# Kernel optimization log

Hardware: AMD Instinct MI355X
Metric: run time of the kernel (lower is better)

Reference implementation:

```python
import jax, jax.numpy as jnp
import numpy as np

NUM_ELEMENTS = 100
EMBED_DIM = 256
HIDDEN_DIM = 512
NUM_HEADS = 8
NUM_MASKS = 1
NUM_GAUSSIANS = 50
RBF_RADIUS = 12.0
N_NODES = 20000
N_EDGES = 400000


def setup_inputs() -> dict:
    key = jax.random.key(0)
    ks = jax.random.split(key, 10)
    anum = jax.random.randint(ks[0], (N_NODES,), 0, NUM_ELEMENTS)
    edge_index = jax.random.randint(ks[1], (2, N_EDGES), 0, N_NODES)
    edge_to_src = jax.random.randint(ks[2], (N_EDGES,), 0, N_EDGES)
    dist = jax.random.uniform(ks[3], (N_EDGES,), jnp.float32) * RBF_RADIUS
    # learned parameters (init scales follow reset_parameters)
    emb_table = jax.random.normal(ks[4], (NUM_ELEMENTS ** 2, EMBED_DIM), jnp.float32)
    s_gate = np.sqrt(3.0 / 2.50663)
    gate_W = jax.random.uniform(ks[5], (HIDDEN_DIM, NUM_GAUSSIANS), jnp.float32, -s_gate, s_gate)
    in_dim = EMBED_DIM + NUM_GAUSSIANS
    s_emb = np.sqrt(3.0 / EMBED_DIM)
    W_emb = jax.random.uniform(ks[6], (HIDDEN_DIM, EMBED_DIM), jnp.float32, -s_emb, s_emb)
    W_rbf = jax.random.uniform(ks[7], (HIDDEN_DIM, NUM_GAUSSIANS), jnp.float32, -s_gate, s_gate)
    W_in = jnp.concatenate([W_emb, W_rbf], axis=1)  # [H, emb+G]
    b_in = jnp.zeros((HIDDEN_DIM,), jnp.float32)
    s_out = np.sqrt(1.0 / HIDDEN_DIM)
    W_out = jax.random.uniform(ks[8], (NUM_HEADS * NUM_MASKS, HIDDEN_DIM), jnp.float32, -s_out, s_out)
    b_out = jnp.zeros((NUM_HEADS * NUM_MASKS,), jnp.float32)
    return {"anum": anum, "edge_index": edge_index, "edge_to_src": edge_to_src,
            "dist": dist, "emb_table": emb_table, "gate_W": gate_W,
            "W_in": W_in, "b_in": b_in, "W_out": W_out, "b_out": b_out}


def _gaussian_smearing(dist):
    offset = jnp.linspace(0.0, RBF_RADIUS, NUM_GAUSSIANS, dtype=dist.dtype)
    coeff = -0.5 / (offset[1] - offset[0]) ** 2
    d = dist[:, None] - offset[None, :]  # [E, G]
    return jnp.exp(coeff * d * d)


def reference(anum, edge_index, edge_to_src, dist, emb_table, gate_W, W_in, b_in, W_out, b_out):
    rbf = _gaussian_smearing(dist)                                  # [E, G]
    pair_idx = anum[edge_index[0]] + NUM_ELEMENTS * anum[edge_index[1]]  # [E]
    emb = emb_table[pair_idx]                                       # [E, D]
    x = jnp.concatenate([emb[edge_to_src], rbf], axis=-1)           # [E, D+G]
    gate = rbf @ gate_W.T                                           # [E, H]
    h = jax.nn.silu(x @ W_in.T + b_in) * gate                       # gated ResMLP hidden
    att_bias = h @ W_out.T + b_out                                  # [E, heads*masks]
    att_bias = att_bias.reshape(dist.shape[0], NUM_HEADS, NUM_MASKS)
    return jnp.transpose(att_bias, (2, 1, 0))                       # [masks, heads, E]
```

## Files before the change

kernel.cpp:

```cpp
#include <hip/hip_runtime.h>
#include <hip/hip_bf16.h>

typedef unsigned short u16;
typedef unsigned int   uint;
typedef __attribute__((ext_vector_type(8))) short bf16x8;
typedef __attribute__((ext_vector_type(4))) float f32x4;

constexpr int NELEM = 100;
constexpr int EMBED = 256;
constexpr int HID   = 512;
constexpr int KX    = 306;
constexpr int G     = 50;
constexpr int M     = 64;
constexpr int THREADS = 512;

constexpr int WB_ELEMS = 32 * 10 * 64 * 8;
constexpr int GB_ELEMS = 32 * 2 * 64 * 8;
constexpr int OB_ELEMS = 16 * 64 * 8;
constexpr int WEIGHT_ELEMS = WB_ELEMS + GB_ELEMS + OB_ELEMS;
constexpr int NPREP = WEIGHT_ELEMS / THREADS;

__device__ __forceinline__ u16 f2bf(float x) {
    uint u = __float_as_uint(x);
    u = (u + 0x7fffu + ((u >> 16) & 1u)) >> 16;
    return (u16)u;
}
__device__ __forceinline__ uint pk2(float a, float b) {
    __hip_bfloat162 h = __float22bfloat162_rn(make_float2(a, b));
    return *reinterpret_cast<uint*>(&h);
}
__device__ __forceinline__ float bflo(uint u) { return __uint_as_float(u << 16); }
__device__ __forceinline__ float bfhi(uint u) { return __uint_as_float(u & 0xffff0000u); }
__device__ __forceinline__ float silu(float p) {
    return p * __builtin_amdgcn_rcpf(1.f + __expf(-p));
}
__device__ __forceinline__ f32x4 mfma16(bf16x8 a, bf16x8 b, f32x4 c) {
    return __builtin_amdgcn_mfma_f32_16x16x32_bf16(a, b, c, 0, 0, 0);
}

__global__ __launch_bounds__(THREADS)
void prep_hist_kernel(const float* __restrict__ W_in,
                      const float* __restrict__ gate_W,
                      const float* __restrict__ W_out,
                      const float* __restrict__ b_in,
                      const int* __restrict__ anum,
                      const int* __restrict__ edge_index,
                      const int* __restrict__ edge_to_src,
                      u16* __restrict__ Wb,
                      u16* __restrict__ Gb,
                      u16* __restrict__ Ob,
                      u16* __restrict__ pairids,
                      int* __restrict__ bins,
                      int E) {
    const int bid = blockIdx.x;
    const int t   = threadIdx.x;

    if (bid < NPREP) {
        int idx = bid * THREADS + t;
        if (idx < WB_ELEMS) {
            int j = idx & 7, lane = (idx >> 3) & 63, kn = idx >> 9;
            int ks = kn % 10, nt = kn / 10;
            int h = nt * 16 + (lane & 15);
            int k = ks * 32 + (lane >> 4) * 8 + j;
            float v = (k < KX) ? W_in[h * KX + k] : ((k == KX) ? b_in[h] : 0.f);
            Wb[idx] = f2bf(v);
        } else if (idx < WB_ELEMS + GB_ELEMS) {
            int i2 = idx - WB_ELEMS;
            int j = i2 & 7, lane = (i2 >> 3) & 63, kn = i2 >> 9;
            int ks = kn & 1, nt = kn >> 1;
            int h = nt * 16 + (lane & 15);
            int g = ks * 32 + (lane >> 4) * 8 + j;
            Gb[i2] = f2bf((g < G) ? gate_W[h * G + g] : 0.f);
        } else {
            int i2 = idx - WB_ELEMS - GB_ELEMS;
            int j = i2 & 7, lane = (i2 >> 3) & 63, s = i2 >> 9;
            int m = lane & 15, q = lane >> 4;
            int hid = s * 32 + (j >> 2) * 16 + q * 4 + (j & 3);
            Ob[i2] = f2bf((m < 8) ? W_out[m * HID + hid] : 0.f);
        }
        return;
    }
    int i = (bid - NPREP) * THREADS + t;
    if (i < E) {
        int src  = edge_to_src[i];
        int pair = anum[edge_index[src]] + NELEM * anum[edge_index[E + src]];
        pairids[i] = (u16)pair;
        atomicAdd(&bins[pair], 1);
    }
}

__global__ __launch_bounds__(THREADS)
void scan_kernel(int* __restrict__ bins, int npair) {
    __shared__ int lds[THREADS];
    const int t = threadIdx.x;
    const int chunk = (npair + THREADS - 1) / THREADS;
    const int lo = t * chunk;
    const int hi = min(lo + chunk, npair);
    int s = 0;
    for (int i = lo; i < hi; ++i) s += bins[i];
    lds[t] = s;
    __syncthreads();
    for (int off = 1; off < THREADS; off <<= 1) {
        int add = (t >= off) ? lds[t - off] : 0;
        __syncthreads();
        lds[t] += add;
        __syncthreads();
    }
    int excl = lds[t] - s;
    for (int i = lo; i < hi; ++i) {
        int c = bins[i];
        bins[i] = excl;
        excl += c;
    }
}

__global__ __launch_bounds__(THREADS)
void scatter_hpre_kernel(const float* __restrict__ table,
                         const u16* __restrict__ Wb,
                         const u16* __restrict__ pairids,
                         int* __restrict__ bins,
                         int* __restrict__ perm,
                         u16* __restrict__ spair,
                         float* __restrict__ hpreF,
                         u16*   __restrict__ hpreH,
                         int E, int npair, int nsc, int f32h) {
    __shared__ __align__(16) u16 af[8 * 4 * 64 * 8];
    const int bid = blockIdx.x;
    const int t   = threadIdx.x;

    if (bid < nsc) {
        int i = bid * THREADS + t;
        if (i < E) {
            int p   = pairids[i];
            int pos = atomicAdd(&bins[p], 1);
            perm[pos]  = i;
            spair[pos] = (u16)p;
        }
        return;
    }

    const int pb = bid - nsc;
    const int p0 = pb * M;
    const int wave = t >> 6, lane = t & 63;
    const int col = lane & 15, quad = lane >> 4;

    #pragma unroll
    for (int mt = 0; mt < 4; ++mt) {
        int p = p0 + mt * 16 + col;
        uint4 w = {0u, 0u, 0u, 0u};
        if (p < npair) {
            const float* s = table + (size_t)p * EMBED + wave * 32 + quad * 8;
            float4 v0 = ((const float4*)s)[0], v1 = ((const float4*)s)[1];
            w.x = pk2(v0.x, v0.y); w.y = pk2(v0.z, v0.w);
            w.z = pk2(v1.x, v1.y); w.w = pk2(v1.z, v1.w);
        }
        *(uint4*)&af[((wave * 4 + mt) * 64 + lane) * 8] = w;
    }
    __syncthreads();

    const f32x4 z4 = {0.f, 0.f, 0.f, 0.f};
    #pragma unroll
    for (int nh = 0; nh < 2; ++nh) {
        f32x4 acc[2][4];
        #pragma unroll
        for (int ntl = 0; ntl < 2; ++ntl)
            #pragma unroll
            for (int mt = 0; mt < 4; ++mt) acc[ntl][mt] = z4;
        #pragma unroll 2
        for (int ks = 0; ks < 8; ++ks) {
            bf16x8 a[4];
            #pragma unroll
            for (int mt = 0; mt < 4; ++mt)
                a[mt] = *(const bf16x8*)&af[((ks * 4 + mt) * 64 + lane) * 8];
            #pragma unroll
            for (int ntl = 0; ntl < 2; ++ntl) {
                int ntg = wave * 4 + nh * 2 + ntl;
                bf16x8 wf = *(const bf16x8*)&Wb[((ntg * 10 + ks) * 64 + lane) * 8];
                #pragma unroll
                for (int mt = 0; mt < 4; ++mt)
                    acc[ntl][mt] = mfma16(wf, a[mt], acc[ntl][mt]);
            }
        }
        #pragma unroll
        for (int ntl = 0; ntl < 2; ++ntl)
            #pragma unroll
            for (int mt = 0; mt < 4; ++mt) {
                int p = p0 + mt * 16 + col;
                if (p < npair) {
                    int hb = (wave * 4 + nh * 2 + ntl) * 16 + quad * 4;
                    if (f32h) {
                        *(f32x4*)(hpreF + (size_t)p * HID + hb) = acc[ntl][mt];
                    } else {
                        uint2 o;
                        o.x = pk2(acc[ntl][mt][0], acc[ntl][mt][1]);
                        o.y = pk2(acc[ntl][mt][2], acc[ntl][mt][3]);
                        *(uint2*)(hpreH + (size_t)p * HID + hb) = o;
                    }
                }
            }
    }
}

template <bool F32H>
__global__ __launch_bounds__(THREADS, 4)
void pair_embed_srt(const int* __restrict__ perm,
                    const u16* __restrict__ spair,
                    const float* __restrict__ dist,
                    const float* __restrict__ hpreF,
                    const u16*   __restrict__ hpreH,
                    const float* __restrict__ b_out,
                    const u16* __restrict__ Wb,
                    const u16* __restrict__ Gb,
                    const u16* __restrict__ Ob,
                    float* __restrict__ out,
                    int E) {
    __shared__ __align__(16) u16 smem[16384];
    __shared__ int   rowbase[M];
    __shared__ float dste[M];
    __shared__ int   oidx[M];
    u16*   afrag = smem;
    float* redf  = (float*)smem;

    const int t  = threadIdx.x;
    const int e0 = blockIdx.x * M;
    const int wave = t >> 6, lane = t & 63;
    const int col = lane & 15, quad = lane >> 4;

    if (t < M) {
        int slot = e0 + t;
        int pair = 0, orig = 0; float d = 0.f;
        if (slot < E) {
            orig = perm[slot];
            pair = spair[slot];
            d    = dist[orig];
        }
        rowbase[t] = pair * HID;
        dste[t]    = d;
        oidx[t]    = orig;
    }
    __syncthreads();

    int rbm[4];
    #pragma unroll
    for (int mt = 0; mt < 4; ++mt) rbm[mt] = rowbase[mt * 16 + col];

    f32x4 hp[2][4];
    uint2 hph[2][4];
    #pragma unroll
    for (int mt = 0; mt < 4; ++mt) {
        int base = rbm[mt] + (wave * 4) * 16 + quad * 4;
        if (F32H) {
            const float* p = hpreF + base;
            hp[0][mt] = *(const f32x4*)p;
            hp[1][mt] = *(const f32x4*)(p + 16);
        } else {
            const u16* p = hpreH + base;
            hph[0][mt] = *(const uint2*)p;
            hph[1][mt] = *(const uint2*)(p + 16);
        }
    }

    {
        const float sp    = 12.0f / 49.0f;
        const float coeff = -0.5f / (sp * sp);
        int ks = wave & 1, mtr = wave >> 1;
        float d  = dste[mtr * 16 + col];
        int   g0 = ks * 32 + quad * 8;
        float f[8];
        #pragma unroll
        for (int j = 0; j < 8; ++j) {
            int g = g0 + j;
            float dd = d - sp * (float)g;
            f[j] = (g < G) ? __expf(coeff * dd * dd) : ((g == G) ? 1.f : 0.f);
        }
        uint4 w;
        w.x = pk2(f[0], f[1]); w.y = pk2(f[2], f[3]);
        w.z = pk2(f[4], f[5]); w.w = pk2(f[6], f[7]);
        *(uint4*)&afrag[((ks * 4 + mtr) * 64 + lane) * 8] = w;
    }
    __syncthreads();

    const f32x4 z4 = {0.f, 0.f, 0.f, 0.f};
    f32x4 oacc[4] = {z4, z4, z4, z4};

    #pragma unroll
    for (int nh = 0; nh < 2; ++nh) {
        if (nh == 1) {
            #pragma unroll
            for (int mt = 0; mt < 4; ++mt) {
                int base = rbm[mt] + (wave * 4 + 2) * 16 + quad * 4;
                if (F32H) {
                    const float* p = hpreF + base;
                    hp[0][mt] = *(const f32x4*)p;
                    hp[1][mt] = *(const f32x4*)(p + 16);
                } else {
                    const u16* p = hpreH + base;
                    hph[0][mt] = *(const uint2*)p;
                    hph[1][mt] = *(const uint2*)(p + 16);
                }
            }
        }
        f32x4 acc[2][4], gacc[2][4];
        #pragma unroll
        for (int ntl = 0; ntl < 2; ++ntl)
            #pragma unroll
            for (int mt = 0; mt < 4; ++mt) {
                gacc[ntl][mt] = z4;
                if (F32H) {
                    acc[ntl][mt] = hp[ntl][mt];
                } else {
                    uint2 v = hph[ntl][mt];
                    f32x4 a = {bflo(v.x), bfhi(v.x), bflo(v.y), bfhi(v.y)};
                    acc[ntl][mt] = a;
                }
            }

        const u16* gb = &Gb[((wave * 4 + nh * 2) * 2 * 64 + lane) * 8];
        const u16* wb = &Wb[(((wave * 4 + nh * 2) * 10 + 8) * 64 + lane) * 8];
        #pragma unroll
        for (int ks = 0; ks < 2; ++ks) {
            bf16x8 a[4];
            #pragma unroll
            for (int mt = 0; mt < 4; ++mt)
                a[mt] = *(const bf16x8*)&afrag[((ks * 4 + mt) * 64 + lane) * 8];
            bf16x8 g0f = *(const bf16x8*)&gb[ks * 512];
            bf16x8 w0f = *(const bf16x8*)&wb[ks * 512];
            bf16x8 g1f = *(const bf16x8*)&gb[1024 + ks * 512];
            bf16x8 w1f = *(const bf16x8*)&wb[5120 + ks * 512];
            #pragma unroll
            for (int mt = 0; mt < 4; ++mt) gacc[0][mt] = mfma16(g0f, a[mt], gacc[0][mt]);
            #pragma unroll
            for (int mt = 0; mt < 4; ++mt) acc[0][mt]  = mfma16(w0f, a[mt], acc[0][mt]);
            #pragma unroll
            for (int mt = 0; mt < 4; ++mt) gacc[1][mt] = mfma16(g1f, a[mt], gacc[1][mt]);
            #pragma unroll
            for (int mt = 0; mt < 4; ++mt) acc[1][mt]  = mfma16(w1f, a[mt], acc[1][mt]);
        }

        bf16x8 obf = *(const bf16x8*)&Ob[(((wave << 1) | nh) * 64 + lane) * 8];
        #pragma unroll
        for (int mt = 0; mt < 4; ++mt) {
            uint4 hq;
            hq.x = pk2(silu(acc[0][mt][0]) * gacc[0][mt][0],
                       silu(acc[0][mt][1]) * gacc[0][mt][1]);
            hq.y = pk2(silu(acc[0][mt][2]) * gacc[0][mt][2],
                       silu(acc[0][mt][3]) * gacc[0][mt][3]);
            hq.z = pk2(silu(acc[1][mt][0]) * gacc[1][mt][0],
                       silu(acc[1][mt][1]) * gacc[1][mt][1]);
            hq.w = pk2(silu(acc[1][mt][2]) * gacc[1][mt][2],
                       silu(acc[1][mt][3]) * gacc[1][mt][3]);
            oacc[mt] = mfma16(obf, *(bf16x8*)&hq, oacc[mt]);
        }
    }
    __syncthreads();

    #pragma unroll
    for (int mt = 0; mt < 4; ++mt)
        *(f32x4*)&redf[((wave * 4 + mt) * 64 + lane) * 4] = oacc[mt];
    __syncthreads();

    {
        int head = t >> 6, el = t & 63;
        int mt = el >> 4, c = el & 15;
        int l  = (head >> 2) * 16 + c;
        int r  = head & 3;
        float s = 0.f;
        #pragma unroll
        for (int w = 0; w < 8; ++w)
            s += redf[((w * 4 + mt) * 64 + l) * 4 + r];
        int slot = e0 + el;
        if (slot < E) out[head * E + oidx[el]] = s + b_out[head];
    }
}

template <bool F32H>
__global__ __launch_bounds__(THREADS, 4)
void pair_embed_pre(const int* __restrict__ anum,
                    const int* __restrict__ edge_index,
                    const int* __restrict__ edge_to_src,
                    const float* __restrict__ dist,
                    const float* __restrict__ hpreF,
                    const u16*   __restrict__ hpreH,
                    const float* __restrict__ b_out,
                    const u16* __restrict__ Wb,
                    const u16* __restrict__ Gb,
                    const u16* __restrict__ Ob,
                    float* __restrict__ out,
                    int E) {
    __shared__ __align__(16) u16 smem[16384];
    __shared__ int   rowbase[M];
    __shared__ float dste[M];
    u16*   afrag = smem;
    float* redf  = (float*)smem;

    const int t  = threadIdx.x;
    const int e0 = blockIdx.x * M;
    const int wave = t >> 6, lane = t & 63;
    const int col = lane & 15, quad = lane >> 4;

    if (t < M) {
        int eg = e0 + t;
        int pair = 0; float d = 0.f;
        if (eg < E) {
            int src = edge_to_src[eg];
            pair = anum[edge_index[src]] + NELEM * anum[edge_index[E + src]];
            d = dist[eg];
        }
        rowbase[t] = pair * HID;
        dste[t]    = d;
    }
    __syncthreads();

    int rbm[4];
    #pragma unroll
    for (int mt = 0; mt < 4; ++mt) rbm[mt] = rowbase[mt * 16 + col];

    f32x4 hp[2][4];
    uint2 hph[2][4];
    #pragma unroll
    for (int mt = 0; mt < 4; ++mt) {
        int base = rbm[mt] + (wave * 4) * 16 + quad * 4;
        if (F32H) {
            const float* p = hpreF + base;
            hp[0][mt] = *(const f32x4*)p;
            hp[1][mt] = *(const f32x4*)(p + 16);
        } else {
            const u16* p = hpreH + base;
            hph[0][mt] = *(const uint2*)p;
            hph[1][mt] = *(const uint2*)(p + 16);
        }
    }

    {
        const float sp    = 12.0f / 49.0f;
        const float coeff = -0.5f / (sp * sp);
        int ks = wave & 1, mtr = wave >> 1;
        float d  = dste[mtr * 16 + col];
        int   g0 = ks * 32 + quad * 8;
        float f[8];
        #pragma unroll
        for (int j = 0; j < 8; ++j) {
            int g = g0 + j;
            float dd = d - sp * (float)g;
            f[j] = (g < G) ? __expf(coeff * dd * dd) : ((g == G) ? 1.f : 0.f);
        }
        uint4 w;
        w.x = pk2(f[0], f[1]); w.y = pk2(f[2], f[3]);
        w.z = pk2(f[4], f[5]); w.w = pk2(f[6], f[7]);
        *(uint4*)&afrag[((ks * 4 + mtr) * 64 + lane) * 8] = w;
    }
    __syncthreads();

    const f32x4 z4 = {0.f, 0.f, 0.f, 0.f};
    f32x4 oacc[4] = {z4, z4, z4, z4};

    #pragma unroll
    for (int nh = 0; nh < 2; ++nh) {
        if (nh == 1) {
            #pragma unroll
            for (int mt = 0; mt < 4; ++mt) {
                int base = rbm[mt] + (wave * 4 + 2) * 16 + quad * 4;
                if (F32H) {
                    const float* p = hpreF + base;
                    hp[0][mt] = *(const f32x4*)p;
                    hp[1][mt] = *(const f32x4*)(p + 16);
                } else {
                    const u16* p = hpreH + base;
                    hph[0][mt] = *(const uint2*)p;
                    hph[1][mt] = *(const uint2*)(p + 16);
                }
            }
        }
        f32x4 acc[2][4], gacc[2][4];
        #pragma unroll
        for (int ntl = 0; ntl < 2; ++ntl)
            #pragma unroll
            for (int mt = 0; mt < 4; ++mt) {
                gacc[ntl][mt] = z4;
                if (F32H) {
                    acc[ntl][mt] = hp[ntl][mt];
                } else {
                    uint2 v = hph[ntl][mt];
                    f32x4 a = {bflo(v.x), bfhi(v.x), bflo(v.y), bfhi(v.y)};
                    acc[ntl][mt] = a;
                }
            }

        const u16* gb = &Gb[((wave * 4 + nh * 2) * 2 * 64 + lane) * 8];
        const u16* wb = &Wb[(((wave * 4 + nh * 2) * 10 + 8) * 64 + lane) * 8];
        #pragma unroll
        for (int ks = 0; ks < 2; ++ks) {
            bf16x8 a[4];
            #pragma unroll
            for (int mt = 0; mt < 4; ++mt)
                a[mt] = *(const bf16x8*)&afrag[((ks * 4 + mt) * 64 + lane) * 8];
            bf16x8 g0f = *(const bf16x8*)&gb[ks * 512];
            bf16x8 w0f = *(const bf16x8*)&wb[ks * 512];
            bf16x8 g1f = *(const bf16x8*)&gb[1024 + ks * 512];
            bf16x8 w1f = *(const bf16x8*)&wb[5120 + ks * 512];
            #pragma unroll
            for (int mt = 0; mt < 4; ++mt) gacc[0][mt] = mfma16(g0f, a[mt], gacc[0][mt]);
            #pragma unroll
            for (int mt = 0; mt < 4; ++mt) acc[0][mt]  = mfma16(w0f, a[mt], acc[0][mt]);
            #pragma unroll
            for (int mt = 0; mt < 4; ++mt) gacc[1][mt] = mfma16(g1f, a[mt], gacc[1][mt]);
            #pragma unroll
            for (int mt = 0; mt < 4; ++mt) acc[1][mt]  = mfma16(w1f, a[mt], acc[1][mt]);
        }

        bf16x8 obf = *(const bf16x8*)&Ob[(((wave << 1) | nh) * 64 + lane) * 8];
        #pragma unroll
        for (int mt = 0; mt < 4; ++mt) {
            uint4 hq;
            hq.x = pk2(silu(acc[0][mt][0]) * gacc[0][mt][0],
                       silu(acc[0][mt][1]) * gacc[0][mt][1]);
            hq.y = pk2(silu(acc[0][mt][2]) * gacc[0][mt][2],
                       silu(acc[0][mt][3]) * gacc[0][mt][3]);
            hq.z = pk2(silu(acc[1][mt][0]) * gacc[1][mt][0],
                       silu(acc[1][mt][1]) * gacc[1][mt][1]);
            hq.w = pk2(silu(acc[1][mt][2]) * gacc[1][mt][2],
                       silu(acc[1][mt][3]) * gacc[1][mt][3]);
            oacc[mt] = mfma16(obf, *(bf16x8*)&hq, oacc[mt]);
        }
    }
    __syncthreads();

    #pragma unroll
    for (int mt = 0; mt < 4; ++mt)
        *(f32x4*)&redf[((wave * 4 + mt) * 64 + lane) * 4] = oacc[mt];
    __syncthreads();

    {
        int head = t >> 6, el = t & 63;
        int mt = el >> 4, c = el & 15;
        int l  = (head >> 2) * 16 + c;
        int r  = head & 3;
        float s = 0.f;
        #pragma unroll
        for (int w = 0; w < 8; ++w)
            s += redf[((w * 4 + mt) * 64 + l) * 4 + r];
        int eg = e0 + el;
        if (eg < E) out[head * E + eg] = s + b_out[head];
    }
}

extern "C" void kernel_launch(void* const* d_in, const int* in_sizes, int n_in,
                              void* d_out, int out_size, void* d_ws, size_t ws_size,
                              hipStream_t stream) {
    const int*   anum        = (const int*)d_in[0];
    const int*   edge_index  = (const int*)d_in[1];
    const int*   edge_to_src = (const int*)d_in[2];
    const float* dist        = (const float*)d_in[3];
    const float* emb_table   = (const float*)d_in[4];
    const float* gate_W      = (const float*)d_in[5];
    const float* W_in        = (const float*)d_in[6];
    const float* b_in        = (const float*)d_in[7];
    const float* W_out       = (const float*)d_in[8];
    const float* b_out       = (const float*)d_in[9];
    const int E     = in_sizes[3];
    const int TBL   = in_sizes[4];
    const int NPAIR = TBL / EMBED;

    u16* Wb = (u16*)d_ws;
    u16* Gb = Wb + WB_ELEMS;
    u16* Ob = Gb + GB_ELEMS;
    const size_t WSW  = (size_t)WEIGHT_ELEMS * 2;
    const size_t hb32 = (size_t)NPAIR * HID * 4;
    const size_t hb16 = (size_t)NPAIR * HID * 2;
    const size_t sortx = (size_t)E * 8 + (size_t)NPAIR * 4;

    int mode;
    if      (ws_size >= WSW + hb32 + sortx) mode = 4;
    else if (ws_size >= WSW + hb16 + sortx) mode = 3;
    else if (ws_size >= WSW + hb32)         mode = 2;
    else                                    mode = 1;

    const size_t hb = (mode == 4 || mode == 2) ? hb32 : hb16;
    char*  hbase   = (char*)d_ws + WSW;
    float* hpreF   = (float*)hbase;
    u16*   hpreH   = (u16*)hbase;
    char*  q       = hbase + hb;
    int*   perm    = (int*)q;
    u16*   pairids = (u16*)(q + (size_t)E * 4);
    u16*   spair   = (u16*)(q + (size_t)E * 6);
    int*   bins    = (int*)(q + (size_t)E * 8);

    const int nhist   = (E + THREADS - 1) / THREADS;
    const int npb     = (NPAIR + M - 1) / M;
    const int nblocks = (E + M - 1) / M;
    const int f32h    = (mode == 4 || mode == 2) ? 1 : 0;

    if (mode >= 3) {
        hipMemsetAsync(bins, 0, (size_t)NPAIR * 4, stream);
        prep_hist_kernel<<<NPREP + nhist, THREADS, 0, stream>>>(
            W_in, gate_W, W_out, b_in, anum, edge_index, edge_to_src,
            Wb, Gb, Ob, pairids, bins, E);
        scan_kernel<<<1, THREADS, 0, stream>>>(bins, NPAIR);
        scatter_hpre_kernel<<<nhist + npb, THREADS, 0, stream>>>(
            emb_table, Wb, pairids, bins, perm, spair, hpreF, hpreH,
            E, NPAIR, nhist, f32h);
        if (mode == 4) {
            pair_embed_srt<true><<<nblocks, THREADS, 0, stream>>>(
                perm, spair, dist, hpreF, hpreH, b_out, Wb, Gb, Ob, (float*)d_out, E);
        } else {
            pair_embed_srt<false><<<nblocks, THREADS, 0, stream>>>(
                perm, spair, dist, hpreF, hpreH, b_out, Wb, Gb, Ob, (float*)d_out, E);
        }
    } else {
        prep_hist_kernel<<<NPREP, THREADS, 0, stream>>>(
            W_in, gate_W, W_out, b_in, anum, edge_index, edge_to_src,
            Wb, Gb, Ob, pairids, bins, E);
        scatter_hpre_kernel<<<npb, THREADS, 0, stream>>>(
            emb_table, Wb, pairids, bins, perm, spair, hpreF, hpreH,
            E, NPAIR, 0, f32h);
        if (mode == 2) {
            pair_embed_pre<true><<<nblocks, THREADS, 0, stream>>>(
                anum, edge_index, edge_to_src, dist, hpreF, hpreH,
                b_out, Wb, Gb, Ob, (float*)d_out, E);
        } else {
            pair_embed_pre<false><<<nblocks, THREADS, 0, stream>>>(
                anum, edge_index, edge_to_src, dist, hpreF, hpreH,
                b_out, Wb, Gb, Ob, (float*)d_out, E);
        }
    }
}
```

Before: 293.2 us.

## Scatter sorted distances and permute outputs in a separate coalesced pass

In the scatter pass the kernel now records each edge's sorted position and writes its distance into sorted order. The main kernel therefore reads spair and sdist contiguously instead of gathering perm and dist. The main kernel writes its results to a sorted-order scratch buffer. A new permute kernel then gathers those rows and writes the head-major output with coalesced stores, replacing the scattered per-head writes. The bf16 hpre fallback paths are removed. This costs an extra kernel launch, a scratch buffer of E*32 bytes, and extra traffic for the round trip through that buffer.

```diff
diff --git a/kernel.cpp b/kernel.cpp
--- a/kernel.cpp
+++ b/kernel.cpp
@@ -29,8 +29,6 @@
     __hip_bfloat162 h = __float22bfloat162_rn(make_float2(a, b));
     return *reinterpret_cast<uint*>(&h);
 }
-__device__ __forceinline__ float bflo(uint u) { return __uint_as_float(u << 16); }
-__device__ __forceinline__ float bfhi(uint u) { return __uint_as_float(u & 0xffff0000u); }
 __device__ __forceinline__ float silu(float p) {
     return p * __builtin_amdgcn_rcpf(1.f + __expf(-p));
 }
@@ -118,12 +116,13 @@
 void scatter_hpre_kernel(const float* __restrict__ table,
                          const u16* __restrict__ Wb,
                          const u16* __restrict__ pairids,
+                         const float* __restrict__ dist,
                          int* __restrict__ bins,
-                         int* __restrict__ perm,
+                         int* __restrict__ ip,
                          u16* __restrict__ spair,
+                         float* __restrict__ sdist,
                          float* __restrict__ hpreF,
-                         u16*   __restrict__ hpreH,
-                         int E, int npair, int nsc, int f32h) {
+                         int E, int npair, int nsc, int mode_a) {
     __shared__ __align__(16) u16 af[8 * 4 * 64 * 8];
     const int bid = blockIdx.x;
     const int t   = threadIdx.x;
@@ -133,7 +132,12 @@
         if (i < E) {
             int p   = pairids[i];
             int pos = atomicAdd(&bins[p], 1);
-            perm[pos]  = i;
+            if (mode_a) {
+                ip[i]      = pos;
+                sdist[pos] = dist[i];
+            } else {
+                ip[pos] = i;
+            }
             spair[pos] = (u16)p;
         }
         return;
@@ -188,36 +192,25 @@
                 int p = p0 + mt * 16 + col;
                 if (p < npair) {
                     int hb = (wave * 4 + nh * 2 + ntl) * 16 + quad * 4;
-                    if (f32h) {
-                        *(f32x4*)(hpreF + (size_t)p * HID + hb) = acc[ntl][mt];
-                    } else {
-                        uint2 o;
-                        o.x = pk2(acc[ntl][mt][0], acc[ntl][mt][1]);
-                        o.y = pk2(acc[ntl][mt][2], acc[ntl][mt][3]);
-                        *(uint2*)(hpreH + (size_t)p * HID + hb) = o;
-                    }
+                    *(f32x4*)(hpreF + (size_t)p * HID + hb) = acc[ntl][mt];
                 }
             }
     }
 }
 
-template <bool F32H>
 __global__ __launch_bounds__(THREADS, 4)
-void pair_embed_srt(const int* __restrict__ perm,
-                    const u16* __restrict__ spair,
-                    const float* __restrict__ dist,
-                    const float* __restrict__ hpreF,
-                    const u16*   __restrict__ hpreH,
-                    const float* __restrict__ b_out,
-                    const u16* __restrict__ Wb,
-                    const u16* __restrict__ Gb,
-                    const u16* __restrict__ Ob,
-                    float* __restrict__ out,
-                    int E) {
+void pair_embed_srtA(const u16* __restrict__ spair,
+                     const float* __restrict__ sdist,
+                     const float* __restrict__ hpreF,
+                     const float* __restrict__ b_out,
+                     const u16* __restrict__ Wb,
+                     const u16* __restrict__ Gb,
+                     const u16* __restrict__ Ob,
+                     float* __restrict__ tmp,
+                     int E) {
     __shared__ __align__(16) u16 smem[16384];
     __shared__ int   rowbase[M];
     __shared__ float dste[M];
-    __shared__ int   oidx[M];
     u16*   afrag = smem;
     float* redf  = (float*)smem;
 
@@ -228,15 +221,10 @@
 
     if (t < M) {
         int slot = e0 + t;
-        int pair = 0, orig = 0; float d = 0.f;
-        if (slot < E) {
-            orig = perm[slot];
-            pair = spair[slot];
-            d    = dist[orig];
-        }
+        int pair = 0; float d = 0.f;
+        if (slot < E) { pair = spair[slot]; d = sdist[slot]; }
         rowbase[t] = pair * HID;
         dste[t]    = d;
-        oidx[t]    = orig;
     }
     __syncthreads();
 
@@ -245,19 +233,11 @@
     for (int mt = 0; mt < 4; ++mt) rbm[mt] = rowbase[mt * 16 + col];
 
     f32x4 hp[2][4];
-    uint2 hph[2][4];
     #pragma unroll
     for (int mt = 0; mt < 4; ++mt) {
-        int base = rbm[mt] + (wave * 4) * 16 + quad * 4;
-        if (F32H) {
-            const float* p = hpreF + base;
-            hp[0][mt] = *(const f32x4*)p;
-            hp[1][mt] = *(const f32x4*)(p + 16);
-        } else {
-            const u16* p = hpreH + base;
-            hph[0][mt] = *(const uint2*)p;
-            hph[1][mt] = *(const uint2*)(p + 16);
-        }
+        const float* p = hpreF + rbm[mt] + (wave * 4) * 16 + quad * 4;
+        hp[0][mt] = *(const f32x4*)p;
+        hp[1][mt] = *(const f32x4*)(p + 16);
     }
 
     {
@@ -288,16 +268,9 @@
         if (nh == 1) {
             #pragma unroll
             for (int mt = 0; mt < 4; ++mt) {
-                int base = rbm[mt] + (wave * 4 + 2) * 16 + quad * 4;
-                if (F32H) {
-                    const float* p = hpreF + base;
-                    hp[0][mt] = *(const f32x4*)p;
-                    hp[1][mt] = *(const f32x4*)(p + 16);
-                } else {
-                    const u16* p = hpreH + base;
-                    hph[0][mt] = *(const uint2*)p;
-                    hph[1][mt] = *(const uint2*)(p + 16);
-                }
+                const float* p = hpreF + rbm[mt] + (wave * 4 + 2) * 16 + quad * 4;
+                hp[0][mt] = *(const f32x4*)p;
+                hp[1][mt] = *(const f32x4*)(p + 16);
             }
         }
         f32x4 acc[2][4], gacc[2][4];
@@ -306,13 +279,7 @@
             #pragma unroll
             for (int mt = 0; mt < 4; ++mt) {
                 gacc[ntl][mt] = z4;
-                if (F32H) {
-                    acc[ntl][mt] = hp[ntl][mt];
-                } else {
-                    uint2 v = hph[ntl][mt];
-                    f32x4 a = {bflo(v.x), bfhi(v.x), bflo(v.y), bfhi(v.y)};
-                    acc[ntl][mt] = a;
-                }
+                acc[ntl][mt]  = hp[ntl][mt];
             }
 
         const u16* gb = &Gb[((wave * 4 + nh * 2) * 2 * 64 + lane) * 8];
@@ -360,6 +327,171 @@
     __syncthreads();
 
     {
+        int el = t >> 3, head = t & 7;
+        int mt = el >> 4, c = el & 15;
+        int l  = (head >> 2) * 16 + c;
+        int r  = head & 3;
+        float s = 0.f;
+        #pragma unroll
+        for (int w = 0; w < 8; ++w)
+            s += redf[((w * 4 + mt) * 64 + l) * 4 + r];
+        int slot = e0 + el;
+        if (slot < E) tmp[slot * 8 + head] = s + b_out[head];
+    }
+}
+
+__global__ __launch_bounds__(256)
+void permute_out_kernel(const int* __restrict__ iperm,
+                        const float* __restrict__ tmp,
+                        float* __restrict__ out, int E) {
+    int e = blockIdx.x * 256 + threadIdx.x;
+    if (e < E) {
+        int s8 = iperm[e] * 8;
+        f32x4 v0 = *(const f32x4*)(tmp + s8);
+        f32x4 v1 = *(const f32x4*)(tmp + s8 + 4);
+        #pragma unroll
+        for (int h = 0; h < 4; ++h) out[h * E + e] = v0[h];
+        #pragma unroll
+        for (int h = 0; h < 4; ++h) out[(h + 4) * E + e] = v1[h];
+    }
+}
+
+__global__ __launch_bounds__(THREADS, 4)
+void pair_embed_srtB(const int* __restrict__ perm,
+                     const u16* __restrict__ spair,
+                     const float* __restrict__ dist,
+                     const float* __restrict__ hpreF,
+                     const float* __restrict__ b_out,
+                     const u16* __restrict__ Wb,
+                     const u16* __restrict__ Gb,
+                     const u16* __restrict__ Ob,
+                     float* __restrict__ out,
+                     int E) {
+    __shared__ __align__(16) u16 smem[16384];
+    __shared__ int   rowbase[M];
+    __shared__ float dste[M];
+    __shared__ int   oidx[M];
+    u16*   afrag = smem;
+    float* redf  = (float*)smem;
+
+    const int t  = threadIdx.x;
+    const int e0 = blockIdx.x * M;
+    const int wave = t >> 6, lane = t & 63;
+    const int col = lane & 15, quad = lane >> 4;
+
+    if (t < M) {
+        int slot = e0 + t;
+        int pair = 0, orig = 0; float d = 0.f;
+        if (slot < E) {
+            orig = perm[slot];
+            pair = spair[slot];
+            d    = dist[orig];
+        }
+        rowbase[t] = pair * HID;
+        dste[t]    = d;
+        oidx[t]    = orig;
+    }
+    __syncthreads();
+
+    int rbm[4];
+    #pragma unroll
+    for (int mt = 0; mt < 4; ++mt) rbm[mt] = rowbase[mt * 16 + col];
+
+    f32x4 hp[2][4];
+    #pragma unroll
+    for (int mt = 0; mt < 4; ++mt) {
+        const float* p = hpreF + rbm[mt] + (wave * 4) * 16 + quad * 4;
+        hp[0][mt] = *(const f32x4*)p;
+        hp[1][mt] = *(const f32x4*)(p + 16);
+    }
+
+    {
+        const float sp    = 12.0f / 49.0f;
+        const float coeff = -0.5f / (sp * sp);
+        int ks = wave & 1, mtr = wave >> 1;
+        float d  = dste[mtr * 16 + col];
+        int   g0 = ks * 32 + quad * 8;
+        float f[8];
+        #pragma unroll
+        for (int j = 0; j < 8; ++j) {
+            int g = g0 + j;
+            float dd = d - sp * (float)g;
+            f[j] = (g < G) ? __expf(coeff * dd * dd) : ((g == G) ? 1.f : 0.f);
+        }
+        uint4 w;
+        w.x = pk2(f[0], f[1]); w.y = pk2(f[2], f[3]);
+        w.z = pk2(f[4], f[5]); w.w = pk2(f[6], f[7]);
+        *(uint4*)&afrag[((ks * 4 + mtr) * 64 + lane) * 8] = w;
+    }
+    __syncthreads();
+
+    const f32x4 z4 = {0.f, 0.f, 0.f, 0.f};
+    f32x4 oacc[4] = {z4, z4, z4, z4};
+
+    #pragma unroll
+    for (int nh = 0; nh < 2; ++nh) {
+        if (nh == 1) {
+            #pragma unroll
+            for (int mt = 0; mt < 4; ++mt) {
+                const float* p = hpreF + rbm[mt] + (wave * 4 + 2) * 16 + quad * 4;
+                hp[0][mt] = *(const f32x4*)p;
+                hp[1][mt] = *(const f32x4*)(p + 16);
+            }
+        }
+        f32x4 acc[2][4], gacc[2][4];
+        #pragma unroll
+        for (int ntl = 0; ntl < 2; ++ntl)
+            #pragma unroll
+            for (int mt = 0; mt < 4; ++mt) {
+                gacc[ntl][mt] = z4;
+                acc[ntl][mt]  = hp[ntl][mt];
+            }
+
+        const u16* gb = &Gb[((wave * 4 + nh * 2) * 2 * 64 + lane) * 8];
+        const u16* wb = &Wb[(((wave * 4 + nh * 2) * 10 + 8) * 64 + lane) * 8];
+        #pragma unroll
+        for (int ks = 0; ks < 2; ++ks) {
+            bf16x8 a[4];
+            #pragma unroll
+            for (int mt = 0; mt < 4; ++mt)
+                a[mt] = *(const bf16x8*)&afrag[((ks * 4 + mt) * 64 + lane) * 8];
+            bf16x8 g0f = *(const bf16x8*)&gb[ks * 512];
+            bf16x8 w0f = *(const bf16x8*)&wb[ks * 512];
+            bf16x8 g1f = *(const bf16x8*)&gb[1024 + ks * 512];
+            bf16x8 w1f = *(const bf16x8*)&wb[5120 + ks * 512];
+            #pragma unroll
+            for (int mt = 0; mt < 4; ++mt) gacc[0][mt] = mfma16(g0f, a[mt], gacc[0][mt]);
+            #pragma unroll
+            for (int mt = 0; mt < 4; ++mt) acc[0][mt]  = mfma16(w0f, a[mt], acc[0][mt]);
+            #pragma unroll
+            for (int mt = 0; mt < 4; ++mt) gacc[1][mt] = mfma16(g1f, a[mt], gacc[1][mt]);
+            #pragma unroll
+            for (int mt = 0; mt < 4; ++mt) acc[1][mt]  = mfma16(w1f, a[mt], acc[1][mt]);
+        }
+
+        bf16x8 obf = *(const bf16x8*)&Ob[(((wave << 1) | nh) * 64 + lane) * 8];
+        #pragma unroll
+        for (int mt = 0; mt < 4; ++mt) {
+            uint4 hq;
+            hq.x = pk2(silu(acc[0][mt][0]) * gacc[0][mt][0],
+                       silu(acc[0][mt][1]) * gacc[0][mt][1]);
+            hq.y = pk2(silu(acc[0][mt][2]) * gacc[0][mt][2],
+                       silu(acc[0][mt][3]) * gacc[0][mt][3]);
+            hq.z = pk2(silu(acc[1][mt][0]) * gacc[1][mt][0],
+                       silu(acc[1][mt][1]) * gacc[1][mt][1]);
+            hq.w = pk2(silu(acc[1][mt][2]) * gacc[1][mt][2],
+                       silu(acc[1][mt][3]) * gacc[1][mt][3]);
+            oacc[mt] = mfma16(obf, *(bf16x8*)&hq, oacc[mt]);
+        }
+    }
+    __syncthreads();
+
+    #pragma unroll
+    for (int mt = 0; mt < 4; ++mt)
+        *(f32x4*)&redf[((wave * 4 + mt) * 64 + lane) * 4] = oacc[mt];
+    __syncthreads();
+
+    {
         int head = t >> 6, el = t & 63;
         int mt = el >> 4, c = el & 15;
         int l  = (head >> 2) * 16 + c;
@@ -373,20 +505,18 @@
     }
 }
 
-template <bool F32H>
 __global__ __launch_bounds__(THREADS, 4)
-void pair_embed_pre(const int* __restrict__ anum,
-                    const int* __restrict__ edge_index,
-                    const int* __restrict__ edge_to_src,
-                    const float* __restrict__ dist,
-                    const float* __restrict__ hpreF,
-                    const u16*   __restrict__ hpreH,
-                    const float* __restrict__ b_out,
-                    const u16* __restrict__ Wb,
-                    const u16* __restrict__ Gb,
-                    const u16* __restrict__ Ob,
-                    float* __restrict__ out,
-                    int E) {
+void pair_embed_unsrt(const int* __restrict__ anum,
+                      const int* __restrict__ edge_index,
+                      const int* __restrict__ edge_to_src,
+                      const float* __restrict__ dist,
+                      const float* __restrict__ hpreF,
+                      const float* __restrict__ b_out,
+                      const u16* __restrict__ Wb,
+                      const u16* __restrict__ Gb,
+                      const u16* __restrict__ Ob,
+                      float* __restrict__ out,
+                      int E) {
     __shared__ __align__(16) u16 smem[16384];
     __shared__ int   rowbase[M];
     __shared__ float dste[M];
@@ -416,19 +546,11 @@
     for (int mt = 0; mt < 4; ++mt) rbm[mt] = rowbase[mt * 16 + col];
 
     f32x4 hp[2][4];
-    uint2 hph[2][4];
     #pragma unroll
     for (int mt = 0; mt < 4; ++mt) {
-        int base = rbm[mt] + (wave * 4) * 16 + quad * 4;
-        if (F32H) {
-            const float* p = hpreF + base;
-            hp[0][mt] = *(const f32x4*)p;
-            hp[1][mt] = *(const f32x4*)(p + 16);
-        } else {
-            const u16* p = hpreH + base;
-            hph[0][mt] = *(const uint2*)p;
-            hph[1][mt] = *(const uint2*)(p + 16);
-        }
+        const float* p = hpreF + rbm[mt] + (wave * 4) * 16 + quad * 4;
+        hp[0][mt] = *(const f32x4*)p;
+        hp[1][mt] = *(const f32x4*)(p + 16);
     }
 
     {
@@ -459,16 +581,9 @@
         if (nh == 1) {
             #pragma unroll
             for (int mt = 0; mt < 4; ++mt) {
-                int base = rbm[mt] + (wave * 4 + 2) * 16 + quad * 4;
-                if (F32H) {
-                    const float* p = hpreF + base;
-                    hp[0][mt] = *(const f32x4*)p;
-                    hp[1][mt] = *(const f32x4*)(p + 16);
-                } else {
-                    const u16* p = hpreH + base;
-                    hph[0][mt] = *(const uint2*)p;
-                    hph[1][mt] = *(const uint2*)(p + 16);
-                }
+                const float* p = hpreF + rbm[mt] + (wave * 4 + 2) * 16 + quad * 4;
+                hp[0][mt] = *(const f32x4*)p;
+                hp[1][mt] = *(const f32x4*)(p + 16);
             }
         }
         f32x4 acc[2][4], gacc[2][4];
@@ -477,13 +592,7 @@
             #pragma unroll
             for (int mt = 0; mt < 4; ++mt) {
                 gacc[ntl][mt] = z4;
-                if (F32H) {
-                    acc[ntl][mt] = hp[ntl][mt];
-                } else {
-                    uint2 v = hph[ntl][mt];
-                    f32x4 a = {bflo(v.x), bfhi(v.x), bflo(v.y), bfhi(v.y)};
-                    acc[ntl][mt] = a;
-                }
+                acc[ntl][mt]  = hp[ntl][mt];
             }
 
         const u16* gb = &Gb[((wave * 4 + nh * 2) * 2 * 64 + lane) * 8];
@@ -565,62 +674,56 @@
     u16* Gb = Wb + WB_ELEMS;
     u16* Ob = Gb + GB_ELEMS;
     const size_t WSW  = (size_t)WEIGHT_ELEMS * 2;
-    const size_t hb32 = (size_t)NPAIR * HID * 4;
-    const size_t hb16 = (size_t)NPAIR * HID * 2;
-    const size_t sortx = (size_t)E * 8 + (size_t)NPAIR * 4;
-
-    int mode;
-    if      (ws_size >= WSW + hb32 + sortx) mode = 4;
-    else if (ws_size >= WSW + hb16 + sortx) mode = 3;
-    else if (ws_size >= WSW + hb32)         mode = 2;
-    else                                    mode = 1;
-
-    const size_t hb = (mode == 4 || mode == 2) ? hb32 : hb16;
+    const size_t HB   = (size_t)NPAIR * HID * 4;
+    const size_t TMPB = (size_t)E * 32;
+    const size_t SRTA = (size_t)E * 12 + (size_t)NPAIR * 4;
+    const size_t SRTB = (size_t)E * 8  + (size_t)NPAIR * 4;
+
+    const size_t szA = WSW + HB + TMPB + SRTA;
+    const size_t szB = WSW + HB + SRTB;
+    const int mode = (ws_size >= szA) ? 2 : ((ws_size >= szB) ? 1 : 0);
+
     char*  hbase   = (char*)d_ws + WSW;
     float* hpreF   = (float*)hbase;
-    u16*   hpreH   = (u16*)hbase;
-    char*  q       = hbase + hb;
-    int*   perm    = (int*)q;
+    float* tmp     = (float*)(hbase + HB);
+    char*  q       = hbase + HB + ((mode == 2) ? TMPB : 0);
+    int*   ip      = (int*)q;
     u16*   pairids = (u16*)(q + (size_t)E * 4);
     u16*   spair   = (u16*)(q + (size_t)E * 6);
-    int*   bins    = (int*)(q + (size_t)E * 8);
+    float* sdist   = (float*)(q + (size_t)E * 8);
+    int*   bins    = (int*)(q + (size_t)E * ((mode == 2) ? 12 : 8));
 
     const int nhist   = (E + THREADS - 1) / THREADS;
     const int npb     = (NPAIR + M - 1) / M;
     const int nblocks = (E + M - 1) / M;
-    const int f32h    = (mode == 4 || mode == 2) ? 1 : 0;
-
-    if (mode >= 3) {
+
+    if (mode >= 1) {
         hipMemsetAsync(bins, 0, (size_t)NPAIR * 4, stream);
         prep_hist_kernel<<<NPREP + nhist, THREADS, 0, stream>>>(
             W_in, gate_W, W_out, b_in, anum, edge_index, edge_to_src,
             Wb, Gb, Ob, pairids, bins, E);
         scan_kernel<<<1, THREADS, 0, stream>>>(bins, NPAIR);
         scatter_hpre_kernel<<<nhist + npb, THREADS, 0, stream>>>(
-            emb_table, Wb, pairids, bins, perm, spair, hpreF, hpreH,
-            E, NPAIR, nhist, f32h);
-        if (mode == 4) {
-            pair_embed_srt<true><<<nblocks, THREADS, 0, stream>>>(
-                perm, spair, dist, hpreF, hpreH, b_out, Wb, Gb, Ob, (float*)d_out, E);
+            emb_table, Wb, pairids, dist, bins, ip, spair, sdist, hpreF,
+            E, NPAIR, nhist, (mode == 2) ? 1 : 0);
+        if (mode == 2) {
+            pair_embed_srtA<<<nblocks, THREADS, 0, stream>>>(
+                spair, sdist, hpreF, b_out, Wb, Gb, Ob, tmp, E);
+            permute_out_kernel<<<(E + 255) / 256, 256, 0, stream>>>(
+                ip, tmp, (float*)d_out, E);
         } else {
-            pair_embed_srt<false><<<nblocks, THREADS, 0, stream>>>(
-                perm, spair, dist, hpreF, hpreH, b_out, Wb, Gb, Ob, (float*)d_out, E);
+            pair_embed_srtB<<<nblocks, THREADS, 0, stream>>>(
+                ip, spair, dist, hpreF, b_out, Wb, Gb, Ob, (float*)d_out, E);
         }
     } else {
         prep_hist_kernel<<<NPREP, THREADS, 0, stream>>>(
             W_in, gate_W, W_out, b_in, anum, edge_index, edge_to_src,
             Wb, Gb, Ob, pairids, bins, E);
         scatter_hpre_kernel<<<npb, THREADS, 0, stream>>>(
-            emb_table, Wb, pairids, bins, perm, spair, hpreF, hpreH,
-            E, NPAIR, 0, f32h);
-        if (mode == 2) {
-            pair_embed_pre<true><<<nblocks, THREADS, 0, stream>>>(
-                anum, edge_index, edge_to_src, dist, hpreF, hpreH,
-                b_out, Wb, Gb, Ob, (float*)d_out, E);
-        } else {
-            pair_embed_pre<false><<<nblocks, THREADS, 0, stream>>>(
-                anum, edge_index, edge_to_src, dist, hpreF, hpreH,
-                b_out, Wb, Gb, Ob, (float*)d_out, E);
-        }
-    }
-}
+            emb_table, Wb, pairids, dist, bins, ip, spair, sdist, hpreF,
+            E, NPAIR, 0, 0);
+        pair_embed_unsrt<<<nblocks, THREADS, 0, stream>>>(
+            anum, edge_index, edge_to_src, dist, hpreF, b_out,
+            Wb, Gb, Ob, (float*)d_out, E);
+    }
+}
```

Result: no change. 295.3 us (+0.7%).
